# Performance work log

Hardware: AMD Instinct MI355X
Metric: run time of the kernel (lower is better)

The kernel has to match this reference:

```python
import jax, jax.numpy as jnp
import numpy as np
from math import sqrt

H = 8          # num_heads
ROPE_BASE = 10000.0


def _rotate_half_interleaved(t):
    # rearrange '... (dim r) -> r ... dim' with r=2 then stack [-x2, x1] back interleaved
    x1 = t[..., 0::2]
    x2 = t[..., 1::2]
    return jnp.stack([-x2, x1], axis=-1).reshape(t.shape)


def _apply_rope(t, pos):
    # t: [B,H,L,W] with W even; pos: [L]
    W = t.shape[-1]
    theta = 1.0 / (ROPE_BASE ** (jnp.arange(0, W, 2, dtype=jnp.float32) / W))  # [W/2]
    m_theta = pos[:, None].astype(jnp.float32) * theta[None, :]                 # [L,W/2]
    m_theta = jnp.repeat(m_theta, 2, axis=-1)                                   # [L,W]
    cos = jnp.cos(m_theta)
    sin = jnp.sin(m_theta)
    return cos * t + sin * _rotate_half_interleaved(t)


def setup_inputs() -> dict:
    key = jax.random.key(0)
    ks = jax.random.split(key, 7)
    B, L, D = 2, 2048, 512
    s = 0.05
    return {
        'x': jax.random.normal(ks[0], (B, L, D), jnp.float32),
        'Wq': jax.random.normal(ks[1], (D, D), jnp.float32) * s,
        'bq': jnp.zeros((D,), jnp.float32),
        'Wk': jax.random.normal(ks[2], (D, D), jnp.float32) * s,
        'bk': jnp.zeros((D,), jnp.float32),
        'Wv': jax.random.normal(ks[3], (D, D), jnp.float32) * s,
        'bv': jnp.zeros((D,), jnp.float32),
        'Wo': jax.random.normal(ks[4], (D, D), jnp.float32) * s,
        'bo': jnp.zeros((D,), jnp.float32),
        'bias_emb': jax.random.normal(ks[5], (2, H), jnp.float32) * s,
        'n_vars': 32,
        'n_tokens': 64,
    }


def reference(x, Wq, bq, Wk, bk, Wv, bv, Wo, bo, bias_emb, n_vars, n_tokens):
    B, L, D = x.shape
    E = D // H  # head_dim
    # q/k/v projections (nn.Linear: x @ W.T + b)
    q = (x @ Wq.T + bq).reshape(B, L, H, E).transpose(0, 2, 1, 3)  # [B,H,L,E]
    k = (x @ Wk.T + bk).reshape(B, L, H, E).transpose(0, 2, 1, 3)  # [B,H,L,E]
    v = (x @ Wv.T + bv).reshape(B, L, H, E)                        # [B,S,H,E]

    # partial RoPE on first half of head_dim (partial_factor=(0.0, 0.5))
    half = E // 2
    pos = jnp.arange(L)
    q = jnp.concatenate([_apply_rope(q[..., :half], pos), q[..., half:]], axis=-1)
    k = jnp.concatenate([_apply_rope(k[..., :half], pos), k[..., half:]], axis=-1)

    # binary attention bias by same-variable indicator
    idx = jnp.arange(L)
    vid = idx // n_tokens
    tid = idx % n_tokens
    same_var = vid[:, None] == vid[None, :]                         # [L,L]
    bias = jnp.where(same_var[None], bias_emb[1][:, None, None],
                     bias_emb[0][:, None, None])                    # [H,L,L]

    # TimerCovariateMask: allow same-variable causal; last n_tokens queries
    # may also attend to all earlier keys
    allowed = same_var & (tid[None, :] <= tid[:, None])
    last_rows = idx >= (L - n_tokens)
    early_cols = idx < (L - n_tokens)
    blocked = (~allowed) & ~(last_rows[:, None] & early_cols[None, :])
    attn_mask = jnp.where(blocked[None], -jnp.inf, bias)            # [H,L,L]

    scale = 1.0 / sqrt(E)
    scores = jnp.einsum('bhle,bhse->bhls', q, k) + attn_mask[None]  # [B,H,L,L]
    A = jax.nn.softmax(scale * scores, axis=-1)
    Vout = jnp.einsum('bhls,bshd->blhd', A, v)                      # [B,L,H,E]
    out = Vout.reshape(B, L, H * E) @ Wo.T + bo                     # [B,L,D]
    return out
```

## Files before the change

kernel.cpp:

```cpp
#include <hip/hip_runtime.h>

typedef __attribute__((ext_vector_type(8))) short short8;
typedef __attribute__((ext_vector_type(4))) float f32x4;
typedef __attribute__((ext_vector_type(4))) unsigned short u16x4;

#define MFMA16(a, b, c) __builtin_amdgcn_mfma_f32_16x16x32_bf16(a, b, c, 0, 0, 0)

__device__ __forceinline__ unsigned short f2bf(float f) {
    union { float f; unsigned int u; } v; v.f = f;
    unsigned int r = (v.u + 0x7fffu + ((v.u >> 16) & 1u)) >> 16;
    return (unsigned short)r;
}
__device__ __forceinline__ float bf2f(unsigned short h) {
    union { unsigned int u; float f; } v; v.u = ((unsigned int)h) << 16;
    return v.f;
}

__global__ __launch_bounds__(256) void convertk(
    const float* __restrict__ x, const float* __restrict__ wq,
    const float* __restrict__ wk, const float* __restrict__ wv,
    const float* __restrict__ wo, unsigned short* __restrict__ xb,
    unsigned short* __restrict__ wb)
{
    int i = (blockIdx.x * 256 + threadIdx.x) * 4;
    const float* src;
    unsigned short* dst;
    if (i < 2097152) { src = x + i; dst = xb + i; }
    else {
        int j = i - 2097152;
        int w = j >> 18;
        int o = j & 262143;
        src = (w == 0 ? wq : w == 1 ? wk : w == 2 ? wv : wo) + o;
        dst = wb + j;
    }
    float4 v = *(const float4*)src;
    u16x4 p;
    p[0] = f2bf(v.x); p[1] = f2bf(v.y); p[2] = f2bf(v.z); p[3] = f2bf(v.w);
    *(u16x4*)dst = p;
}

__global__ __launch_bounds__(256) void gemm_qkv(
    const unsigned short* __restrict__ xb, const unsigned short* __restrict__ wb,
    const float* __restrict__ bq, const float* __restrict__ bk,
    const float* __restrict__ bv,
    unsigned short* __restrict__ qb, unsigned short* __restrict__ kb,
    unsigned short* __restrict__ vT)
{
    const int z = blockIdx.z;
    const unsigned short* Wz = wb + z * 262144;
    const int n0 = blockIdx.x * 128, m0 = blockIdx.y * 128;
    __shared__ unsigned short Al[128 * 40];
    __shared__ unsigned short Bl[128 * 40];
    const int t = threadIdx.x;
    const int lane = t & 63, w = t >> 6;
    const int wm = (w >> 1) * 64, wn = (w & 1) * 64;
    const int quad = lane >> 4, n16 = lane & 15;
    const int rs = t >> 2, cs = (t & 3) * 8;
    f32x4 acc[4][4] = {};
    for (int k0 = 0; k0 < 512; k0 += 32) {
        __syncthreads();
        *(short8*)&Al[rs * 40 + cs]        = *(const short8*)&xb[(m0 + rs) * 512 + k0 + cs];
        *(short8*)&Al[(rs + 64) * 40 + cs] = *(const short8*)&xb[(m0 + rs + 64) * 512 + k0 + cs];
        *(short8*)&Bl[rs * 40 + cs]        = *(const short8*)&Wz[(n0 + rs) * 512 + k0 + cs];
        *(short8*)&Bl[(rs + 64) * 40 + cs] = *(const short8*)&Wz[(n0 + rs + 64) * 512 + k0 + cs];
        __syncthreads();
        short8 af[4], bf[4];
        #pragma unroll
        for (int i = 0; i < 4; i++)
            af[i] = *(const short8*)&Al[(wm + i * 16 + n16) * 40 + quad * 8];
        #pragma unroll
        for (int i = 0; i < 4; i++)
            bf[i] = *(const short8*)&Bl[(wn + i * 16 + n16) * 40 + quad * 8];
        #pragma unroll
        for (int mi = 0; mi < 4; mi++)
            #pragma unroll
            for (int ni = 0; ni < 4; ni++)
                acc[mi][ni] = MFMA16(af[mi], bf[ni], acc[mi][ni]);
    }
    const float* bias_p = (z == 0) ? bq : (z == 1) ? bk : bv;
    unsigned short* dst01 = (z == 0) ? qb : kb;
    #pragma unroll
    for (int mi = 0; mi < 4; mi++) {
        #pragma unroll
        for (int ni = 0; ni < 4; ni++) {
            const int n = n0 + wn + ni * 16 + n16;
            const int mb = m0 + wm + mi * 16 + quad * 4;
            const float bias = bias_p[n];
            const int h = n >> 6, e = n & 63;
            f32x4 v = acc[mi][ni];
            if (z < 2) {
                #pragma unroll
                for (int r = 0; r < 4; r++) {
                    int m = mb + r, b = m >> 11, l = m & 2047;
                    dst01[((b * 8 + h) * 2048 + l) * 64 + e] = f2bf(v[r] + bias);
                }
            } else {
                int b = mb >> 11, l = mb & 2047;
                u16x4 pk;
                #pragma unroll
                for (int r = 0; r < 4; r++) pk[r] = f2bf(v[r] + bias);
                *(u16x4*)&vT[((b * 8 + h) * 64 + e) * 2048 + l] = pk;
            }
        }
    }
}

__global__ __launch_bounds__(256) void ropek(unsigned short* __restrict__ qb,
                                             unsigned short* __restrict__ kb)
{
    int i = blockIdx.x * 256 + threadIdx.x;
    int j = i & 15;
    int l = (i >> 4) & 2047;
    int bh = (i >> 15) & 15;
    int which = i >> 19;
    unsigned short* p = which ? kb : qb;
    int base = (bh * 2048 + l) * 64 + 2 * j;
    float t0 = bf2f(p[base]), t1 = bf2f(p[base + 1]);
    float theta = expf(-(float)j * 0.5756462732485115f);
    float ang = (float)l * theta;
    float s = sinf(ang), c = cosf(ang);
    p[base]     = f2bf(c * t0 - s * t1);
    p[base + 1] = f2bf(c * t1 + s * t0);
}

__global__ __launch_bounds__(256) void attn_diag(
    const unsigned short* __restrict__ qb, const unsigned short* __restrict__ kb,
    const unsigned short* __restrict__ vT, const float* __restrict__ bias_emb,
    unsigned short* __restrict__ voutb)
{
    const int var = blockIdx.x, h = blockIdx.y, b = blockIdx.z;
    const int t = threadIdx.x, lane = t & 63, w = t >> 6;
    const int quad = lane >> 4, n16 = lane & 15;
    const int bh = b * 8 + h;
    const int m0 = var * 64 + w * 16;
    __shared__ unsigned short Pl[4 * 1280];
    unsigned short* Pw = &Pl[w * 1280];
    const int qoff = bh * 2048 * 64;
    const float scale = 0.125f;
    const float bias_same = bias_emb[8 + h];
    const int iloc = w * 16 + quad * 4;
    const int j0 = var * 64;

    short8 aq0 = *(const short8*)&qb[qoff + (m0 + n16) * 64 + quad * 8];
    short8 aq1 = *(const short8*)&qb[qoff + (m0 + n16) * 64 + 32 + quad * 8];

    f32x4 sc[4];
    #pragma unroll
    for (int nt = 0; nt < 4; nt++) {
        short8 k0f = *(const short8*)&kb[qoff + (j0 + nt * 16 + n16) * 64 + quad * 8];
        short8 k1f = *(const short8*)&kb[qoff + (j0 + nt * 16 + n16) * 64 + 32 + quad * 8];
        f32x4 s = {};
        s = MFMA16(aq0, k0f, s);
        s = MFMA16(aq1, k1f, s);
        sc[nt] = s;
    }
    float zl[4][4];
    #pragma unroll
    for (int nt = 0; nt < 4; nt++) {
        int jloc = nt * 16 + n16;
        #pragma unroll
        for (int r = 0; r < 4; r++) {
            float zz = scale * (sc[nt][r] + bias_same);
            if (jloc > iloc + r) zz = -1e30f;
            zl[nt][r] = zz;
        }
    }
    float cm[4], rsum[4], pr[4][4];
    #pragma unroll
    for (int r = 0; r < 4; r++)
        cm[r] = fmaxf(fmaxf(zl[0][r], zl[1][r]), fmaxf(zl[2][r], zl[3][r]));
    #pragma unroll
    for (int off = 1; off < 16; off <<= 1)
        #pragma unroll
        for (int r = 0; r < 4; r++)
            cm[r] = fmaxf(cm[r], __shfl_xor(cm[r], off));
    #pragma unroll
    for (int nt = 0; nt < 4; nt++)
        #pragma unroll
        for (int r = 0; r < 4; r++)
            pr[nt][r] = __expf(zl[nt][r] - cm[r]);
    #pragma unroll
    for (int r = 0; r < 4; r++)
        rsum[r] = (pr[0][r] + pr[1][r]) + (pr[2][r] + pr[3][r]);
    #pragma unroll
    for (int off = 1; off < 16; off <<= 1)
        #pragma unroll
        for (int r = 0; r < 4; r++)
            rsum[r] += __shfl_xor(rsum[r], off);
    #pragma unroll
    for (int nt = 0; nt < 4; nt++) {
        int s = nt >> 1, c = (nt & 1) * 16 + n16;
        #pragma unroll
        for (int r = 0; r < 4; r++)
            Pw[s * 640 + (quad * 4 + r) * 40 + c] = f2bf(pr[nt][r]);
    }
    short8 pa0 = *(const short8*)&Pw[0 * 640 + n16 * 40 + quad * 8];
    short8 pa1 = *(const short8*)&Pw[1 * 640 + n16 * 40 + quad * 8];
    f32x4 oacc[4] = {};
    #pragma unroll
    for (int et = 0; et < 4; et++) {
        const int vrow = (bh * 64 + et * 16 + n16) * 2048;
        short8 v0 = *(const short8*)&vT[vrow + j0 + quad * 8];
        short8 v1 = *(const short8*)&vT[vrow + j0 + 32 + quad * 8];
        oacc[et] = MFMA16(pa0, v0, oacc[et]);
        oacc[et] = MFMA16(pa1, v1, oacc[et]);
    }
    #pragma unroll
    for (int et = 0; et < 4; et++) {
        #pragma unroll
        for (int r = 0; r < 4; r++) {
            float o = oacc[et][r] / rsum[r];
            int l = m0 + quad * 4 + r;
            voutb[(b * 2048 + l) * 512 + h * 64 + et * 16 + n16] = f2bf(o);
        }
    }
}

__global__ __launch_bounds__(256) void attn31(
    const unsigned short* __restrict__ qb, const unsigned short* __restrict__ kb,
    const unsigned short* __restrict__ vT, const float* __restrict__ bias_emb,
    float* __restrict__ Opart, float* __restrict__ Mp, float* __restrict__ Lp)
{
    const int split = blockIdx.x, h = blockIdx.y, b = blockIdx.z;
    const int t = threadIdx.x, lane = t & 63, w = t >> 6;
    const int quad = lane >> 4, n16 = lane & 15;
    const int bh = b * 8 + h;
    const int m0 = 31 * 64 + w * 16;
    __shared__ unsigned short Pl[4 * 1280];
    unsigned short* Pw = &Pl[w * 1280];
    const int qoff = bh * 2048 * 64;
    const float scale = 0.125f;
    const float bias_same = bias_emb[8 + h];
    const float bias_diff = bias_emb[h];
    const int iloc = w * 16 + quad * 4;

    short8 aq0 = *(const short8*)&qb[qoff + (m0 + n16) * 64 + quad * 8];
    short8 aq1 = *(const short8*)&qb[qoff + (m0 + n16) * 64 + 32 + quad * 8];

    f32x4 oacc[4] = {};
    float mrow[4], lrow[4];
    #pragma unroll
    for (int r = 0; r < 4; r++) { mrow[r] = -1e30f; lrow[r] = 0.f; }

    #pragma unroll
    for (int ci = 0; ci < 4; ci++) {
        const int chunk = split * 4 + ci;
        const bool diag = (chunk == 31);
        const float biasv = diag ? bias_same : bias_diff;
        const int j0 = chunk * 64;

        f32x4 sc[4];
        #pragma unroll
        for (int nt = 0; nt < 4; nt++) {
            short8 k0f = *(const short8*)&kb[qoff + (j0 + nt * 16 + n16) * 64 + quad * 8];
            short8 k1f = *(const short8*)&kb[qoff + (j0 + nt * 16 + n16) * 64 + 32 + quad * 8];
            f32x4 s = {};
            s = MFMA16(aq0, k0f, s);
            s = MFMA16(aq1, k1f, s);
            sc[nt] = s;
        }
        float zl[4][4];
        #pragma unroll
        for (int nt = 0; nt < 4; nt++) {
            int jloc = nt * 16 + n16;
            #pragma unroll
            for (int r = 0; r < 4; r++) {
                float zz = scale * (sc[nt][r] + biasv);
                if (diag && jloc > iloc + r) zz = -1e30f;
                zl[nt][r] = zz;
            }
        }
        float cm[4];
        #pragma unroll
        for (int r = 0; r < 4; r++)
            cm[r] = fmaxf(fmaxf(zl[0][r], zl[1][r]), fmaxf(zl[2][r], zl[3][r]));
        #pragma unroll
        for (int off = 1; off < 16; off <<= 1)
            #pragma unroll
            for (int r = 0; r < 4; r++)
                cm[r] = fmaxf(cm[r], __shfl_xor(cm[r], off));
        float mnew[4], alpha[4], rsum[4], pr[4][4];
        #pragma unroll
        for (int r = 0; r < 4; r++) {
            mnew[r] = fmaxf(mrow[r], cm[r]);
            alpha[r] = __expf(mrow[r] - mnew[r]);
        }
        #pragma unroll
        for (int nt = 0; nt < 4; nt++)
            #pragma unroll
            for (int r = 0; r < 4; r++)
                pr[nt][r] = __expf(zl[nt][r] - mnew[r]);
        #pragma unroll
        for (int r = 0; r < 4; r++)
            rsum[r] = (pr[0][r] + pr[1][r]) + (pr[2][r] + pr[3][r]);
        #pragma unroll
        for (int off = 1; off < 16; off <<= 1)
            #pragma unroll
            for (int r = 0; r < 4; r++)
                rsum[r] += __shfl_xor(rsum[r], off);
        #pragma unroll
        for (int r = 0; r < 4; r++) {
            lrow[r] = lrow[r] * alpha[r] + rsum[r];
            mrow[r] = mnew[r];
        }
        #pragma unroll
        for (int et = 0; et < 4; et++)
            #pragma unroll
            for (int r = 0; r < 4; r++)
                oacc[et][r] *= alpha[r];
        #pragma unroll
        for (int nt = 0; nt < 4; nt++) {
            int s = nt >> 1, c = (nt & 1) * 16 + n16;
            #pragma unroll
            for (int r = 0; r < 4; r++)
                Pw[s * 640 + (quad * 4 + r) * 40 + c] = f2bf(pr[nt][r]);
        }
        short8 pa0 = *(const short8*)&Pw[0 * 640 + n16 * 40 + quad * 8];
        short8 pa1 = *(const short8*)&Pw[1 * 640 + n16 * 40 + quad * 8];
        #pragma unroll
        for (int et = 0; et < 4; et++) {
            const int vrow = (bh * 64 + et * 16 + n16) * 2048;
            short8 v0 = *(const short8*)&vT[vrow + j0 + quad * 8];
            short8 v1 = *(const short8*)&vT[vrow + j0 + 32 + quad * 8];
            oacc[et] = MFMA16(pa0, v0, oacc[et]);
            oacc[et] = MFMA16(pa1, v1, oacc[et]);
        }
    }
    const int pb = (bh * 8 + split) * 64;
    #pragma unroll
    for (int et = 0; et < 4; et++)
        #pragma unroll
        for (int r = 0; r < 4; r++)
            Opart[(pb + w * 16 + quad * 4 + r) * 64 + et * 16 + n16] = oacc[et][r];
    if (n16 == 0) {
        #pragma unroll
        for (int r = 0; r < 4; r++) {
            Mp[pb + w * 16 + quad * 4 + r] = mrow[r];
            Lp[pb + w * 16 + quad * 4 + r] = lrow[r];
        }
    }
}

__global__ __launch_bounds__(256) void attn31_merge(
    const float* __restrict__ Opart, const float* __restrict__ Mp,
    const float* __restrict__ Lp, unsigned short* __restrict__ voutb)
{
    const int bh = blockIdx.x, b = bh >> 3, h = bh & 7;
    const int t = threadIdx.x;
    const int row = t >> 2, c0 = (t & 3) * 16;
    float ms[8];
    float M = -1e30f;
    #pragma unroll
    for (int s = 0; s < 8; s++) {
        ms[s] = Mp[(bh * 8 + s) * 64 + row];
        M = fmaxf(M, ms[s]);
    }
    float L = 0.f;
    float es[8];
    #pragma unroll
    for (int s = 0; s < 8; s++) {
        es[s] = __expf(ms[s] - M);
        L += Lp[(bh * 8 + s) * 64 + row] * es[s];
    }
    float acc[16] = {};
    #pragma unroll
    for (int s = 0; s < 8; s++) {
        const float* op = &Opart[((bh * 8 + s) * 64 + row) * 64 + c0];
        #pragma unroll
        for (int k = 0; k < 4; k++) {
            float4 v = *(const float4*)&op[k * 4];
            acc[k*4+0] += v.x * es[s]; acc[k*4+1] += v.y * es[s];
            acc[k*4+2] += v.z * es[s]; acc[k*4+3] += v.w * es[s];
        }
    }
    const float inv = 1.f / L;
    const int l = 31 * 64 + row;
    u16x4 pk;
    #pragma unroll
    for (int k = 0; k < 4; k++) {
        pk[0] = f2bf(acc[k*4+0] * inv); pk[1] = f2bf(acc[k*4+1] * inv);
        pk[2] = f2bf(acc[k*4+2] * inv); pk[3] = f2bf(acc[k*4+3] * inv);
        *(u16x4*)&voutb[(b * 2048 + l) * 512 + h * 64 + c0 + k * 4] = pk;
    }
}

__global__ __launch_bounds__(256) void gemm_out(
    const unsigned short* __restrict__ ab, const unsigned short* __restrict__ wo,
    const float* __restrict__ bo, float* __restrict__ out)
{
    const int n0 = blockIdx.x * 128, m0 = blockIdx.y * 128;
    __shared__ unsigned short Al[128 * 40];
    __shared__ unsigned short Bl[128 * 40];
    const int t = threadIdx.x;
    const int lane = t & 63, w = t >> 6;
    const int wm = (w >> 1) * 64, wn = (w & 1) * 64;
    const int quad = lane >> 4, n16 = lane & 15;
    const int rs = t >> 2, cs = (t & 3) * 8;
    f32x4 acc[4][4] = {};
    for (int k0 = 0; k0 < 512; k0 += 32) {
        __syncthreads();
        *(short8*)&Al[rs * 40 + cs]        = *(const short8*)&ab[(m0 + rs) * 512 + k0 + cs];
        *(short8*)&Al[(rs + 64) * 40 + cs] = *(const short8*)&ab[(m0 + rs + 64) * 512 + k0 + cs];
        *(short8*)&Bl[rs * 40 + cs]        = *(const short8*)&wo[(n0 + rs) * 512 + k0 + cs];
        *(short8*)&Bl[(rs + 64) * 40 + cs] = *(const short8*)&wo[(n0 + rs + 64) * 512 + k0 + cs];
        __syncthreads();
        short8 af[4], bf[4];
        #pragma unroll
        for (int i = 0; i < 4; i++)
            af[i] = *(const short8*)&Al[(wm + i * 16 + n16) * 40 + quad * 8];
        #pragma unroll
        for (int i = 0; i < 4; i++)
            bf[i] = *(const short8*)&Bl[(wn + i * 16 + n16) * 40 + quad * 8];
        #pragma unroll
        for (int mi = 0; mi < 4; mi++)
            #pragma unroll
            for (int ni = 0; ni < 4; ni++)
                acc[mi][ni] = MFMA16(af[mi], bf[ni], acc[mi][ni]);
    }
    #pragma unroll
    for (int mi = 0; mi < 4; mi++) {
        #pragma unroll
        for (int ni = 0; ni < 4; ni++) {
            const int n = n0 + wn + ni * 16 + n16;
            const int mb = m0 + wm + mi * 16 + quad * 4;
            const float bias = bo[n];
            f32x4 v = acc[mi][ni];
            #pragma unroll
            for (int r = 0; r < 4; r++)
                out[(mb + r) * 512 + n] = v[r] + bias;
        }
    }
}

extern "C" void kernel_launch(void* const* d_in, const int* in_sizes, int n_in,
                              void* d_out, int out_size, void* d_ws, size_t ws_size,
                              hipStream_t stream)
{
    const float* x        = (const float*)d_in[0];
    const float* Wq       = (const float*)d_in[1];
    const float* bq       = (const float*)d_in[2];
    const float* Wk       = (const float*)d_in[3];
    const float* bk       = (const float*)d_in[4];
    const float* Wv       = (const float*)d_in[5];
    const float* bv       = (const float*)d_in[6];
    const float* Wo       = (const float*)d_in[7];
    const float* bo       = (const float*)d_in[8];
    const float* bias_emb = (const float*)d_in[9];

    unsigned short* xb  = (unsigned short*)d_ws;
    unsigned short* wb  = xb + 2097152;
    unsigned short* qb  = wb + 1048576;
    unsigned short* kb  = qb + 2097152;
    unsigned short* vT  = kb + 2097152;
    unsigned short* vob = vT + 2097152;

    float* Opart = (float*)xb;
    float* Mp    = Opart + 524288;
    float* Lp    = Mp + 8192;

    hipLaunchKernelGGL(convertk, dim3(3072), dim3(256), 0, stream,
                       x, Wq, Wk, Wv, Wo, xb, wb);
    hipLaunchKernelGGL(gemm_qkv, dim3(4, 32, 3), dim3(256), 0, stream,
                       xb, wb, bq, bk, bv, qb, kb, vT);
    hipLaunchKernelGGL(ropek, dim3(4096), dim3(256), 0, stream, qb, kb);
    hipLaunchKernelGGL(attn_diag, dim3(31, 8, 2), dim3(256), 0, stream,
                       qb, kb, vT, bias_emb, vob);
    hipLaunchKernelGGL(attn31, dim3(8, 8, 2), dim3(256), 0, stream,
                       qb, kb, vT, bias_emb, Opart, Mp, Lp);
    hipLaunchKernelGGL(attn31_merge, dim3(16), dim3(256), 0, stream,
                       Opart, Mp, Lp, vob);
    hipLaunchKernelGGL(gemm_out, dim3(4, 32, 1), dim3(256), 0, stream,
                       vob, wb + 3 * 262144, bo, (float*)d_out);
}
```

Baseline: 140.9 us.

## Fuse RoPE into QKV GEMM epilogue and merge attention kernels into one launch

```diff
diff --git a/kernel.cpp b/kernel.cpp
--- a/kernel.cpp
+++ b/kernel.cpp
@@ -10,10 +10,6 @@
     union { float f; unsigned int u; } v; v.f = f;
     unsigned int r = (v.u + 0x7fffu + ((v.u >> 16) & 1u)) >> 16;
     return (unsigned short)r;
-}
-__device__ __forceinline__ float bf2f(unsigned short h) {
-    union { unsigned int u; float f; } v; v.u = ((unsigned int)h) << 16;
-    return v.f;
 }
 
 __global__ __launch_bounds__(256) void convertk(
@@ -86,169 +82,63 @@
             const int n = n0 + wn + ni * 16 + n16;
             const int mb = m0 + wm + mi * 16 + quad * 4;
             const float bias = bias_p[n];
-            const int h = n >> 6, e = n & 63;
+            const int h = n >> 6, e_lo = ni * 16 + n16;
             f32x4 v = acc[mi][ni];
             if (z < 2) {
+                float vr[4];
+                #pragma unroll
+                for (int r = 0; r < 4; r++) vr[r] = v[r] + bias;
+                if (ni < 2) {
+                    const int j = e_lo >> 1;
+                    const float theta = exp2f(-(float)j * 0.8304820237218405f);
+                    #pragma unroll
+                    for (int r = 0; r < 4; r++) {
+                        int l = (mb + r) & 2047;
+                        float s, c;
+                        __sincosf((float)l * theta, &s, &c);
+                        float p = __shfl_xor(vr[r], 1);
+                        vr[r] = (e_lo & 1) ? (c * vr[r] + s * p) : (c * vr[r] - s * p);
+                    }
+                }
                 #pragma unroll
                 for (int r = 0; r < 4; r++) {
                     int m = mb + r, b = m >> 11, l = m & 2047;
-                    dst01[((b * 8 + h) * 2048 + l) * 64 + e] = f2bf(v[r] + bias);
+                    dst01[((b * 8 + h) * 2048 + l) * 64 + e_lo] = f2bf(vr[r]);
                 }
             } else {
                 int b = mb >> 11, l = mb & 2047;
                 u16x4 pk;
                 #pragma unroll
                 for (int r = 0; r < 4; r++) pk[r] = f2bf(v[r] + bias);
-                *(u16x4*)&vT[((b * 8 + h) * 64 + e) * 2048 + l] = pk;
-            }
-        }
-    }
-}
-
-__global__ __launch_bounds__(256) void ropek(unsigned short* __restrict__ qb,
-                                             unsigned short* __restrict__ kb)
-{
-    int i = blockIdx.x * 256 + threadIdx.x;
-    int j = i & 15;
-    int l = (i >> 4) & 2047;
-    int bh = (i >> 15) & 15;
-    int which = i >> 19;
-    unsigned short* p = which ? kb : qb;
-    int base = (bh * 2048 + l) * 64 + 2 * j;
-    float t0 = bf2f(p[base]), t1 = bf2f(p[base + 1]);
-    float theta = expf(-(float)j * 0.5756462732485115f);
-    float ang = (float)l * theta;
-    float s = sinf(ang), c = cosf(ang);
-    p[base]     = f2bf(c * t0 - s * t1);
-    p[base + 1] = f2bf(c * t1 + s * t0);
-}
-
-__global__ __launch_bounds__(256) void attn_diag(
+                *(u16x4*)&vT[((b * 8 + h) * 64 + e_lo) * 2048 + l] = pk;
+            }
+        }
+    }
+}
+
+__global__ __launch_bounds__(256) void attn_all(
     const unsigned short* __restrict__ qb, const unsigned short* __restrict__ kb,
     const unsigned short* __restrict__ vT, const float* __restrict__ bias_emb,
-    unsigned short* __restrict__ voutb)
-{
-    const int var = blockIdx.x, h = blockIdx.y, b = blockIdx.z;
+    unsigned short* __restrict__ voutb,
+    float* __restrict__ Opart, float* __restrict__ Mp, float* __restrict__ Lp)
+{
+    const int xid = blockIdx.x, h = blockIdx.y, b = blockIdx.z;
     const int t = threadIdx.x, lane = t & 63, w = t >> 6;
     const int quad = lane >> 4, n16 = lane & 15;
     const int bh = b * 8 + h;
-    const int m0 = var * 64 + w * 16;
     __shared__ unsigned short Pl[4 * 1280];
     unsigned short* Pw = &Pl[w * 1280];
     const int qoff = bh * 2048 * 64;
     const float scale = 0.125f;
     const float bias_same = bias_emb[8 + h];
     const int iloc = w * 16 + quad * 4;
-    const int j0 = var * 64;
-
-    short8 aq0 = *(const short8*)&qb[qoff + (m0 + n16) * 64 + quad * 8];
-    short8 aq1 = *(const short8*)&qb[qoff + (m0 + n16) * 64 + 32 + quad * 8];
-
-    f32x4 sc[4];
-    #pragma unroll
-    for (int nt = 0; nt < 4; nt++) {
-        short8 k0f = *(const short8*)&kb[qoff + (j0 + nt * 16 + n16) * 64 + quad * 8];
-        short8 k1f = *(const short8*)&kb[qoff + (j0 + nt * 16 + n16) * 64 + 32 + quad * 8];
-        f32x4 s = {};
-        s = MFMA16(aq0, k0f, s);
-        s = MFMA16(aq1, k1f, s);
-        sc[nt] = s;
-    }
-    float zl[4][4];
-    #pragma unroll
-    for (int nt = 0; nt < 4; nt++) {
-        int jloc = nt * 16 + n16;
-        #pragma unroll
-        for (int r = 0; r < 4; r++) {
-            float zz = scale * (sc[nt][r] + bias_same);
-            if (jloc > iloc + r) zz = -1e30f;
-            zl[nt][r] = zz;
-        }
-    }
-    float cm[4], rsum[4], pr[4][4];
-    #pragma unroll
-    for (int r = 0; r < 4; r++)
-        cm[r] = fmaxf(fmaxf(zl[0][r], zl[1][r]), fmaxf(zl[2][r], zl[3][r]));
-    #pragma unroll
-    for (int off = 1; off < 16; off <<= 1)
-        #pragma unroll
-        for (int r = 0; r < 4; r++)
-            cm[r] = fmaxf(cm[r], __shfl_xor(cm[r], off));
-    #pragma unroll
-    for (int nt = 0; nt < 4; nt++)
-        #pragma unroll
-        for (int r = 0; r < 4; r++)
-            pr[nt][r] = __expf(zl[nt][r] - cm[r]);
-    #pragma unroll
-    for (int r = 0; r < 4; r++)
-        rsum[r] = (pr[0][r] + pr[1][r]) + (pr[2][r] + pr[3][r]);
-    #pragma unroll
-    for (int off = 1; off < 16; off <<= 1)
-        #pragma unroll
-        for (int r = 0; r < 4; r++)
-            rsum[r] += __shfl_xor(rsum[r], off);
-    #pragma unroll
-    for (int nt = 0; nt < 4; nt++) {
-        int s = nt >> 1, c = (nt & 1) * 16 + n16;
-        #pragma unroll
-        for (int r = 0; r < 4; r++)
-            Pw[s * 640 + (quad * 4 + r) * 40 + c] = f2bf(pr[nt][r]);
-    }
-    short8 pa0 = *(const short8*)&Pw[0 * 640 + n16 * 40 + quad * 8];
-    short8 pa1 = *(const short8*)&Pw[1 * 640 + n16 * 40 + quad * 8];
-    f32x4 oacc[4] = {};
-    #pragma unroll
-    for (int et = 0; et < 4; et++) {
-        const int vrow = (bh * 64 + et * 16 + n16) * 2048;
-        short8 v0 = *(const short8*)&vT[vrow + j0 + quad * 8];
-        short8 v1 = *(const short8*)&vT[vrow + j0 + 32 + quad * 8];
-        oacc[et] = MFMA16(pa0, v0, oacc[et]);
-        oacc[et] = MFMA16(pa1, v1, oacc[et]);
-    }
-    #pragma unroll
-    for (int et = 0; et < 4; et++) {
-        #pragma unroll
-        for (int r = 0; r < 4; r++) {
-            float o = oacc[et][r] / rsum[r];
-            int l = m0 + quad * 4 + r;
-            voutb[(b * 2048 + l) * 512 + h * 64 + et * 16 + n16] = f2bf(o);
-        }
-    }
-}
-
-__global__ __launch_bounds__(256) void attn31(
-    const unsigned short* __restrict__ qb, const unsigned short* __restrict__ kb,
-    const unsigned short* __restrict__ vT, const float* __restrict__ bias_emb,
-    float* __restrict__ Opart, float* __restrict__ Mp, float* __restrict__ Lp)
-{
-    const int split = blockIdx.x, h = blockIdx.y, b = blockIdx.z;
-    const int t = threadIdx.x, lane = t & 63, w = t >> 6;
-    const int quad = lane >> 4, n16 = lane & 15;
-    const int bh = b * 8 + h;
-    const int m0 = 31 * 64 + w * 16;
-    __shared__ unsigned short Pl[4 * 1280];
-    unsigned short* Pw = &Pl[w * 1280];
-    const int qoff = bh * 2048 * 64;
-    const float scale = 0.125f;
-    const float bias_same = bias_emb[8 + h];
-    const float bias_diff = bias_emb[h];
-    const int iloc = w * 16 + quad * 4;
-
-    short8 aq0 = *(const short8*)&qb[qoff + (m0 + n16) * 64 + quad * 8];
-    short8 aq1 = *(const short8*)&qb[qoff + (m0 + n16) * 64 + 32 + quad * 8];
-
-    f32x4 oacc[4] = {};
-    float mrow[4], lrow[4];
-    #pragma unroll
-    for (int r = 0; r < 4; r++) { mrow[r] = -1e30f; lrow[r] = 0.f; }
-
-    #pragma unroll
-    for (int ci = 0; ci < 4; ci++) {
-        const int chunk = split * 4 + ci;
-        const bool diag = (chunk == 31);
-        const float biasv = diag ? bias_same : bias_diff;
-        const int j0 = chunk * 64;
-
+
+    if (xid < 31) {
+        const int var = xid;
+        const int m0 = var * 64 + w * 16;
+        const int j0 = var * 64;
+        short8 aq0 = *(const short8*)&qb[qoff + (m0 + n16) * 64 + quad * 8];
+        short8 aq1 = *(const short8*)&qb[qoff + (m0 + n16) * 64 + 32 + quad * 8];
         f32x4 sc[4];
         #pragma unroll
         for (int nt = 0; nt < 4; nt++) {
@@ -265,12 +155,12 @@
             int jloc = nt * 16 + n16;
             #pragma unroll
             for (int r = 0; r < 4; r++) {
-                float zz = scale * (sc[nt][r] + biasv);
-                if (diag && jloc > iloc + r) zz = -1e30f;
+                float zz = scale * (sc[nt][r] + bias_same);
+                if (jloc > iloc + r) zz = -1e30f;
                 zl[nt][r] = zz;
             }
         }
-        float cm[4];
+        float cm[4], rsum[4], pr[4][4];
         #pragma unroll
         for (int r = 0; r < 4; r++)
             cm[r] = fmaxf(fmaxf(zl[0][r], zl[1][r]), fmaxf(zl[2][r], zl[3][r]));
@@ -279,17 +169,11 @@
             #pragma unroll
             for (int r = 0; r < 4; r++)
                 cm[r] = fmaxf(cm[r], __shfl_xor(cm[r], off));
-        float mnew[4], alpha[4], rsum[4], pr[4][4];
-        #pragma unroll
-        for (int r = 0; r < 4; r++) {
-            mnew[r] = fmaxf(mrow[r], cm[r]);
-            alpha[r] = __expf(mrow[r] - mnew[r]);
-        }
         #pragma unroll
         for (int nt = 0; nt < 4; nt++)
             #pragma unroll
             for (int r = 0; r < 4; r++)
-                pr[nt][r] = __expf(zl[nt][r] - mnew[r]);
+                pr[nt][r] = __expf(zl[nt][r] - cm[r]);
         #pragma unroll
         for (int r = 0; r < 4; r++)
             rsum[r] = (pr[0][r] + pr[1][r]) + (pr[2][r] + pr[3][r]);
@@ -299,16 +183,6 @@
             for (int r = 0; r < 4; r++)
                 rsum[r] += __shfl_xor(rsum[r], off);
         #pragma unroll
-        for (int r = 0; r < 4; r++) {
-            lrow[r] = lrow[r] * alpha[r] + rsum[r];
-            mrow[r] = mnew[r];
-        }
-        #pragma unroll
-        for (int et = 0; et < 4; et++)
-            #pragma unroll
-            for (int r = 0; r < 4; r++)
-                oacc[et][r] *= alpha[r];
-        #pragma unroll
         for (int nt = 0; nt < 4; nt++) {
             int s = nt >> 1, c = (nt & 1) * 16 + n16;
             #pragma unroll
@@ -317,6 +191,7 @@
         }
         short8 pa0 = *(const short8*)&Pw[0 * 640 + n16 * 40 + quad * 8];
         short8 pa1 = *(const short8*)&Pw[1 * 640 + n16 * 40 + quad * 8];
+        f32x4 oacc[4] = {};
         #pragma unroll
         for (int et = 0; et < 4; et++) {
             const int vrow = (bh * 64 + et * 16 + n16) * 2048;
@@ -325,18 +200,120 @@
             oacc[et] = MFMA16(pa0, v0, oacc[et]);
             oacc[et] = MFMA16(pa1, v1, oacc[et]);
         }
-    }
-    const int pb = (bh * 8 + split) * 64;
-    #pragma unroll
-    for (int et = 0; et < 4; et++)
-        #pragma unroll
-        for (int r = 0; r < 4; r++)
-            Opart[(pb + w * 16 + quad * 4 + r) * 64 + et * 16 + n16] = oacc[et][r];
-    if (n16 == 0) {
-        #pragma unroll
-        for (int r = 0; r < 4; r++) {
-            Mp[pb + w * 16 + quad * 4 + r] = mrow[r];
-            Lp[pb + w * 16 + quad * 4 + r] = lrow[r];
+        #pragma unroll
+        for (int et = 0; et < 4; et++) {
+            #pragma unroll
+            for (int r = 0; r < 4; r++) {
+                float o = oacc[et][r] / rsum[r];
+                int l = m0 + quad * 4 + r;
+                voutb[(b * 2048 + l) * 512 + h * 64 + et * 16 + n16] = f2bf(o);
+            }
+        }
+    } else {
+        const int split = xid - 31;
+        const int m0 = 31 * 64 + w * 16;
+        const float bias_diff = bias_emb[h];
+        short8 aq0 = *(const short8*)&qb[qoff + (m0 + n16) * 64 + quad * 8];
+        short8 aq1 = *(const short8*)&qb[qoff + (m0 + n16) * 64 + 32 + quad * 8];
+        f32x4 oacc[4] = {};
+        float mrow[4], lrow[4];
+        #pragma unroll
+        for (int r = 0; r < 4; r++) { mrow[r] = -1e30f; lrow[r] = 0.f; }
+        #pragma unroll
+        for (int ci = 0; ci < 4; ci++) {
+            const int chunk = split * 4 + ci;
+            const bool diag = (chunk == 31);
+            const float biasv = diag ? bias_same : bias_diff;
+            const int j0 = chunk * 64;
+            f32x4 sc[4];
+            #pragma unroll
+            for (int nt = 0; nt < 4; nt++) {
+                short8 k0f = *(const short8*)&kb[qoff + (j0 + nt * 16 + n16) * 64 + quad * 8];
+                short8 k1f = *(const short8*)&kb[qoff + (j0 + nt * 16 + n16) * 64 + 32 + quad * 8];
+                f32x4 s = {};
+                s = MFMA16(aq0, k0f, s);
+                s = MFMA16(aq1, k1f, s);
+                sc[nt] = s;
+            }
+            float zl[4][4];
+            #pragma unroll
+            for (int nt = 0; nt < 4; nt++) {
+                int jloc = nt * 16 + n16;
+                #pragma unroll
+                for (int r = 0; r < 4; r++) {
+                    float zz = scale * (sc[nt][r] + biasv);
+                    if (diag && jloc > iloc + r) zz = -1e30f;
+                    zl[nt][r] = zz;
+                }
+            }
+            float cm[4];
+            #pragma unroll
+            for (int r = 0; r < 4; r++)
+                cm[r] = fmaxf(fmaxf(zl[0][r], zl[1][r]), fmaxf(zl[2][r], zl[3][r]));
+            #pragma unroll
+            for (int off = 1; off < 16; off <<= 1)
+                #pragma unroll
+                for (int r = 0; r < 4; r++)
+                    cm[r] = fmaxf(cm[r], __shfl_xor(cm[r], off));
+            float mnew[4], alpha[4], rsum[4], pr[4][4];
+            #pragma unroll
+            for (int r = 0; r < 4; r++) {
+                mnew[r] = fmaxf(mrow[r], cm[r]);
+                alpha[r] = __expf(mrow[r] - mnew[r]);
+            }
+            #pragma unroll
+            for (int nt = 0; nt < 4; nt++)
+                #pragma unroll
+                for (int r = 0; r < 4; r++)
+                    pr[nt][r] = __expf(zl[nt][r] - mnew[r]);
+            #pragma unroll
+            for (int r = 0; r < 4; r++)
+                rsum[r] = (pr[0][r] + pr[1][r]) + (pr[2][r] + pr[3][r]);
+            #pragma unroll
+            for (int off = 1; off < 16; off <<= 1)
+                #pragma unroll
+                for (int r = 0; r < 4; r++)
+                    rsum[r] += __shfl_xor(rsum[r], off);
+            #pragma unroll
+            for (int r = 0; r < 4; r++) {
+                lrow[r] = lrow[r] * alpha[r] + rsum[r];
+                mrow[r] = mnew[r];
+            }
+            #pragma unroll
+            for (int et = 0; et < 4; et++)
+                #pragma unroll
+                for (int r = 0; r < 4; r++)
+                    oacc[et][r] *= alpha[r];
+            #pragma unroll
+            for (int nt = 0; nt < 4; nt++) {
+                int s = nt >> 1, c = (nt & 1) * 16 + n16;
+                #pragma unroll
+                for (int r = 0; r < 4; r++)
+                    Pw[s * 640 + (quad * 4 + r) * 40 + c] = f2bf(pr[nt][r]);
+            }
+            short8 pa0 = *(const short8*)&Pw[0 * 640 + n16 * 40 + quad * 8];
+            short8 pa1 = *(const short8*)&Pw[1 * 640 + n16 * 40 + quad * 8];
+            #pragma unroll
+            for (int et = 0; et < 4; et++) {
+                const int vrow = (bh * 64 + et * 16 + n16) * 2048;
+                short8 v0 = *(const short8*)&vT[vrow + j0 + quad * 8];
+                short8 v1 = *(const short8*)&vT[vrow + j0 + 32 + quad * 8];
+                oacc[et] = MFMA16(pa0, v0, oacc[et]);
+                oacc[et] = MFMA16(pa1, v1, oacc[et]);
+            }
+        }
+        const int pb = (bh * 8 + split) * 64;
+        #pragma unroll
+        for (int et = 0; et < 4; et++)
+            #pragma unroll
+            for (int r = 0; r < 4; r++)
+                Opart[(pb + w * 16 + quad * 4 + r) * 64 + et * 16 + n16] = oacc[et][r];
+        if (n16 == 0) {
+            #pragma unroll
+            for (int r = 0; r < 4; r++) {
+                Mp[pb + w * 16 + quad * 4 + r] = mrow[r];
+                Lp[pb + w * 16 + quad * 4 + r] = lrow[r];
+            }
         }
     }
 }
@@ -462,11 +439,8 @@
                        x, Wq, Wk, Wv, Wo, xb, wb);
     hipLaunchKernelGGL(gemm_qkv, dim3(4, 32, 3), dim3(256), 0, stream,
                        xb, wb, bq, bk, bv, qb, kb, vT);
-    hipLaunchKernelGGL(ropek, dim3(4096), dim3(256), 0, stream, qb, kb);
-    hipLaunchKernelGGL(attn_diag, dim3(31, 8, 2), dim3(256), 0, stream,
-                       qb, kb, vT, bias_emb, vob);
-    hipLaunchKernelGGL(attn31, dim3(8, 8, 2), dim3(256), 0, stream,
-                       qb, kb, vT, bias_emb, Opart, Mp, Lp);
+    hipLaunchKernelGGL(attn_all, dim3(39, 8, 2), dim3(256), 0, stream,
+                       qb, kb, vT, bias_emb, vob, Opart, Mp, Lp);
     hipLaunchKernelGGL(attn31_merge, dim3(16), dim3(256), 0, stream,
                        Opart, Mp, Lp, vob);
     hipLaunchKernelGGL(gemm_out, dim3(4, 32, 1), dim3(256), 0, stream,
```

New measurement: 135.4 us. 1.04x faster.
